# Kernel tuning notes

Hardware: AMD Instinct MI355X
Metric: run time of the kernel (lower is better)

## Reference

```python
import jax, jax.numpy as jnp
import numpy as np

B, S, NI = 8, 1024, 1024      # batch, seq_len, n_inputs
L, H, P = 128, 128, 64        # n_latents, hidden=n_inputs//8, prototype_dim
EPS_PROTO = 1e-4              # self.epsilon
BN_EPS = 1e-5                 # torch BatchNorm1d default eps


def setup_inputs() -> dict:
    key = jax.random.key(0)
    ks = jax.random.split(key, 4)
    return {
        "x": jax.random.normal(ks[0], (B, S, NI), jnp.float32),
        "W1": jax.random.normal(ks[1], (L, H, NI), jnp.float32) * 0.02,
        "b1": jnp.zeros((L, H), jnp.float32),
        "gamma": jnp.ones((L, H), jnp.float32),
        "beta": jnp.zeros((L, H), jnp.float32),
        "run_mean": jnp.zeros((L, H), jnp.float32),
        "run_var": jnp.ones((L, H), jnp.float32),
        "W2": jax.random.normal(ks[2], (L, P, H), jnp.float32) * 0.02,
        "b2": jnp.zeros((L, P), jnp.float32),
        "prototypes": jax.random.normal(ks[3], (L, P), jnp.float32) * 0.02,
    }


def reference(x, W1, b1, gamma, beta, run_mean, run_var, W2, b2, prototypes):
    Bb, Ss, _ = x.shape
    xf = x.reshape(Bb * Ss, NI)                       # [T, NI]
    # grouped first Linear over all latents at once: [T, L, H]
    h = jnp.einsum('ti,lhi->tlh', xf, W1) + b1
    # Dropout is identity in eval; BatchNorm1d in eval mode (running stats)
    h = (h - run_mean) * jax.lax.rsqrt(run_var + BN_EPS) * gamma + beta
    h = jax.nn.relu(h)
    # grouped second Linear: [T, L, P]
    enc = jnp.einsum('tlh,lph->tlp', h, W2) + b2
    # prototype L2-distance activation
    l2s = jnp.sum((enc - prototypes) ** 2, axis=-1)   # [T, L]
    raw = jnp.log((l2s + 1.0) / (l2s + EPS_PROTO))
    act = raw / jnp.log(1.0 / EPS_PROTO) * 300.0 - 100.0
    return act.reshape(Bb, Ss, L)
```

## Files before the change

kernel.cpp:

```cpp
#include <hip/hip_runtime.h>


#define NTOK 8192
#define NI   1024
#define NL   128
#define NH   128
#define NP   64

typedef __bf16 bf16x8 __attribute__((ext_vector_type(8)));
typedef float f32x4 __attribute__((ext_vector_type(4)));
typedef int   i32x4 __attribute__((ext_vector_type(4)));

static __device__ __forceinline__ unsigned short f2bf(float f) {
  union { float f; unsigned int u; } v; v.f = f;
  const unsigned int u = v.u;
  return (unsigned short)((u + 0x7fffu + ((u >> 16) & 1u)) >> 16);
}

__global__ void cvt_f32_bf16(const float* __restrict__ in,
                             unsigned short* __restrict__ out, int n8) {
  const int i = blockIdx.x * blockDim.x + threadIdx.x;
  if (i >= n8) return;
  const float4* p = (const float4*)in;
  const float4 a = p[2 * i], b = p[2 * i + 1];
  unsigned short v[8] __attribute__((aligned(16))) = {
      f2bf(a.x), f2bf(a.y), f2bf(a.z), f2bf(a.w),
      f2bf(b.x), f2bf(b.y), f2bf(b.z), f2bf(b.w)};
  ((uint4*)out)[i] = *(const uint4*)v;
}

__global__ void quant_rows_i8_dual(const float* __restrict__ x,
                                   const float* __restrict__ w1,
                                   signed char* __restrict__ xq,
                                   signed char* __restrict__ w1q,
                                   float* __restrict__ sx,
                                   float* __restrict__ sw) {
  const int row = blockIdx.x * 4 + (threadIdx.x >> 6);
  const int lane = threadIdx.x & 63;
  const float* src;
  unsigned int* dst;
  float* sp;
  if (row < NTOK) {
    src = x + (size_t)row * 1024;
    dst = (unsigned int*)(xq + (size_t)row * 1024);
    sp  = sx + row;
  } else {
    const int r = row - NTOK;
    src = w1 + (size_t)r * 1024;
    dst = (unsigned int*)(w1q + (size_t)r * 1024);
    sp  = sw + r;
  }
  const float4* s4 = (const float4*)src;
  float4 v[4];
  float m = 0.f;
#pragma unroll
  for (int j = 0; j < 4; ++j) {
    v[j] = s4[lane + 64 * j];
    m = fmaxf(m, fmaxf(fmaxf(fabsf(v[j].x), fabsf(v[j].y)),
                       fmaxf(fabsf(v[j].z), fabsf(v[j].w))));
  }
#pragma unroll
  for (int s = 1; s < 64; s <<= 1) m = fmaxf(m, __shfl_xor(m, s));
  m = fmaxf(m, 1e-20f);
  const float inv = 127.0f / m;
  if (lane == 0) *sp = m * (1.0f / 127.0f);
#pragma unroll
  for (int j = 0; j < 4; ++j) {
    const int a = (int)rintf(fminf(127.f, fmaxf(-127.f, v[j].x * inv)));
    const int b = (int)rintf(fminf(127.f, fmaxf(-127.f, v[j].y * inv)));
    const int c = (int)rintf(fminf(127.f, fmaxf(-127.f, v[j].z * inv)));
    const int d = (int)rintf(fminf(127.f, fmaxf(-127.f, v[j].w * inv)));
    dst[lane + 64 * j] = (unsigned)(a & 255) | ((unsigned)(b & 255) << 8) |
                         ((unsigned)(c & 255) << 16) | ((unsigned)(d & 255) << 24);
  }
}

static __device__ __forceinline__ void async16(const void* g, void* l) {
  __builtin_amdgcn_global_load_lds(
      (const __attribute__((address_space(1))) unsigned int*)g,
      (__attribute__((address_space(3))) unsigned int*)l, 16, 0, 0);
}

__global__ __launch_bounds__(256, 3) void proto_fused(
    const signed char* __restrict__ xq,
    const signed char* __restrict__ w1q,
    const unsigned short* __restrict__ w2b,
    const float* __restrict__ sx,
    const float* __restrict__ sw,
    const float* __restrict__ b1,
    const float* __restrict__ gamma, const float* __restrict__ beta,
    const float* __restrict__ rmean, const float* __restrict__ rvar,
    const float* __restrict__ b2,
    const float* __restrict__ protos,
    float* __restrict__ out)
{
  __shared__ __attribute__((aligned(128))) char smem[49152];
  const int tid  = threadIdx.x;
  const int wave = tid >> 6;
  const int lane = tid & 63;
  const int l15  = lane & 15;
  const int l4   = lane >> 4;
  const int wr   = wave >> 1;
  const int wc   = wave & 1;
  const int t0   = blockIdx.x * 128;
  const int lat  = blockIdx.y;

  const int srow  = lane >> 3;
  const int scolb = ((lane & 7) ^ srow) * 16;

  i32x4 acc[4][4] = {};

#pragma unroll
  for (int i = 0; i < 4; ++i) {
    const int r = wave * 4 + i * 16 + (lane >> 4);
    const int c = (lane & 15) ^ (r & 15);
    async16(w2b + (size_t)lat * NP * NH + r * NH + c * 8,
            smem + 32768 + (wave * 64 + i * 256) * 16);
  }

  auto stage = [&](int ks) {
    const int k0 = ks * 128;
#pragma unroll
    for (int j = 0; j < 4; ++j) {
      const int row = wave * 32 + j * 8 + srow;
      async16(xq + (size_t)(t0 + row) * NI + k0 + scolb,
              smem + (wave * 4 + j) * 1024);
      async16(w1q + (size_t)(lat * NH + row) * NI + k0 + scolb,
              smem + 16384 + (wave * 4 + j) * 1024);
    }
  };

  stage(0);
  const int rx = l15 & 7;
  for (int ks = 0; ks < 8; ++ks) {
    __syncthreads();
#pragma unroll
    for (int kk = 0; kk < 2; ++kk) {
      const int koff = ((kk * 4 + l4) ^ rx) << 4;
      i32x4 a[4], b[4];
#pragma unroll
      for (int m = 0; m < 4; ++m)
        a[m] = *(const i32x4*)(smem + (wr * 64 + m * 16 + l15) * 128 + koff);
#pragma unroll
      for (int n = 0; n < 4; ++n)
        b[n] = *(const i32x4*)(smem + 16384 + (wc * 64 + n * 16 + l15) * 128 + koff);
#pragma unroll
      for (int m = 0; m < 4; ++m)
#pragma unroll
        for (int n = 0; n < 4; ++n)
          acc[m][n] = __builtin_amdgcn_mfma_i32_16x16x64_i8(a[m], b[n], acc[m][n], 0, 0, 0);
    }
    __syncthreads();
    if (ks + 1 < 8) stage(ks + 1);
  }

  float sxv[4][4];
#pragma unroll
  for (int m = 0; m < 4; ++m)
#pragma unroll
    for (int r = 0; r < 4; ++r)
      sxv[m][r] = sx[t0 + wr * 64 + m * 16 + l4 * 4 + r];

#pragma unroll
  for (int n = 0; n < 4; ++n) {
    const int hc = wc * 64 + n * 16 + l15;
    const int gi = lat * NH + hc;
    const float sc_ = gamma[gi] * rsqrtf(rvar[gi] + 1e-5f);
    const float Kc  = sw[gi] * sc_;
    const float Cc  = b1[gi] * sc_ + beta[gi] - rmean[gi] * sc_;
    const int cchunk = hc >> 3, cin = (hc & 7) * 2;
#pragma unroll
    for (int m = 0; m < 4; ++m)
#pragma unroll
      for (int r = 0; r < 4; ++r) {
        float v = fmaf((float)acc[m][n][r] * sxv[m][r], Kc, Cc);
        v = v > 0.f ? v : 0.f;
        const int row = wr * 64 + m * 16 + l4 * 4 + r;
        const int pbyte = row * 256 + ((cchunk ^ (l4 * 4 + r)) << 4) + cin;
        *(__bf16*)(smem + pbyte) = (__bf16)v;
      }
  }
  __syncthreads();

  f32x4 acc2[2][4] = {};
#pragma unroll
  for (int kk = 0; kk < 4; ++kk) {
    const int pcsel = kk * 4 + l4;
    bf16x8 a2[2], bw[4];
#pragma unroll
    for (int m = 0; m < 2; ++m) {
      const int row = wave * 32 + m * 16 + l15;
      a2[m] = *(const bf16x8*)(smem + row * 256 + ((pcsel ^ (row & 15)) << 4));
    }
#pragma unroll
    for (int n = 0; n < 4; ++n) {
      const int rp = n * 16 + l15;
      bw[n] = *(const bf16x8*)(smem + 32768 + rp * 256 + ((pcsel ^ (rp & 15)) << 4));
    }
#pragma unroll
    for (int m = 0; m < 2; ++m)
#pragma unroll
      for (int n = 0; n < 4; ++n)
        acc2[m][n] = __builtin_amdgcn_mfma_f32_16x16x32_bf16(a2[m], bw[n], acc2[m][n], 0, 0, 0);
  }

  float pb[4], pp[4];
#pragma unroll
  for (int n = 0; n < 4; ++n) {
    const int p = n * 16 + l15;
    pb[n] = b2[lat * NP + p];
    pp[n] = protos[lat * NP + p];
  }
  const float scale2 = 0.69314718056f * 300.0f / logf(10000.0f);
#pragma unroll
  for (int m = 0; m < 2; ++m)
#pragma unroll
    for (int r = 0; r < 4; ++r) {
      float s = 0.f;
#pragma unroll
      for (int n = 0; n < 4; ++n) {
        const float e = acc2[m][n][r] + pb[n] - pp[n];
        s += e * e;
      }
      s += __shfl_xor(s, 1);
      s += __shfl_xor(s, 2);
      s += __shfl_xor(s, 4);
      s += __shfl_xor(s, 8);
      if (l15 == 0) {
        const float a = (__log2f(s + 1.0f) - __log2f(s + 1e-4f)) * scale2 - 100.0f;
        const int trow = wave * 32 + m * 16 + l4 * 4 + r;
        out[(size_t)(t0 + trow) * NL + lat] = a;
      }
    }
}

extern "C" void kernel_launch(void* const* d_in, const int* in_sizes, int n_in,
                              void* d_out, int out_size, void* d_ws, size_t ws_size,
                              hipStream_t stream) {
  const float* x      = (const float*)d_in[0];
  const float* W1     = (const float*)d_in[1];
  const float* b1     = (const float*)d_in[2];
  const float* gamma  = (const float*)d_in[3];
  const float* beta   = (const float*)d_in[4];
  const float* rmean  = (const float*)d_in[5];
  const float* rvar   = (const float*)d_in[6];
  const float* W2     = (const float*)d_in[7];
  const float* b2     = (const float*)d_in[8];
  const float* protos = (const float*)d_in[9];
  float* out = (float*)d_out;

  char* ws = (char*)d_ws;
  signed char*    xq  = (signed char*)ws;
  signed char*    w1q = (signed char*)(ws + (size_t)8 * 1024 * 1024);
  unsigned short* w2b = (unsigned short*)(ws + (size_t)24 * 1024 * 1024);
  float*          sx  = (float*)(ws + (size_t)26 * 1024 * 1024);
  float*          sw  = (float*)(ws + (size_t)26 * 1024 * 1024 + 64 * 1024);

  quant_rows_i8_dual<<<(NTOK + NL * NH) / 4, 256, 0, stream>>>(x, W1, xq, w1q, sx, sw);
  {
    const int n8w2 = NL * NP * NH / 8;
    cvt_f32_bf16<<<(n8w2 + 255) / 256, 256, 0, stream>>>(W2, w2b, n8w2);
  }

  dim3 grid(NTOK / 128, NL);
  proto_fused<<<grid, 256, 0, stream>>>(xq, w1q, w2b, sx, sw, b1, gamma, beta,
                                        rmean, rvar, b2, protos, out);
}
```

Before: 222.9 us.

## Load W2 directly from global, shrink LDS, remap blocks per XCD

Drops the 16KB LDS staging of W2 and has each lane read W2 bf16 fragments straight from global memory, prefetching one k-step ahead. This cuts shared memory to 32KB so occupancy can rise to 4 blocks per CU, and the launch bound is raised to match. The 2D grid becomes a 1D grid with a swizzle that keeps 16 latents per XCD and groups token tiles, so W1 and x tiles are reused in each XCD's L2. The cost is extra global/L2 traffic for W2 and more register pressure from the prefetch buffers.

```diff
diff --git a/kernel.cpp b/kernel.cpp
--- a/kernel.cpp
+++ b/kernel.cpp
@@ -81,7 +81,7 @@
       (__attribute__((address_space(3))) unsigned int*)l, 16, 0, 0);
 }
 
-__global__ __launch_bounds__(256, 3) void proto_fused(
+__global__ __launch_bounds__(256, 4) void proto_fused(
     const signed char* __restrict__ xq,
     const signed char* __restrict__ w1q,
     const unsigned short* __restrict__ w2b,
@@ -94,7 +94,7 @@
     const float* __restrict__ protos,
     float* __restrict__ out)
 {
-  __shared__ __attribute__((aligned(128))) char smem[49152];
+  __shared__ __attribute__((aligned(128))) char smem[32768];
   const int tid  = threadIdx.x;
   const int wave = tid >> 6;
   const int lane = tid & 63;
@@ -102,21 +102,20 @@
   const int l4   = lane >> 4;
   const int wr   = wave >> 1;
   const int wc   = wave & 1;
-  const int t0   = blockIdx.x * 128;
-  const int lat  = blockIdx.y;
+
+  const int id    = blockIdx.x;
+  const int xcd   = id & 7;
+  const int local = id >> 3;
+  const int chunk = local >> 7;
+  const int wi    = local & 127;
+  const int tt    = chunk * 8 + (wi & 7);
+  const int lat   = xcd * 16 + (wi >> 3);
+  const int t0    = tt * 128;
 
   const int srow  = lane >> 3;
   const int scolb = ((lane & 7) ^ srow) * 16;
 
   i32x4 acc[4][4] = {};
-
-#pragma unroll
-  for (int i = 0; i < 4; ++i) {
-    const int r = wave * 4 + i * 16 + (lane >> 4);
-    const int c = (lane & 15) ^ (r & 15);
-    async16(w2b + (size_t)lat * NP * NH + r * NH + c * 8,
-            smem + 32768 + (wave * 64 + i * 256) * 16);
-  }
 
   auto stage = [&](int ks) {
     const int k0 = ks * 128;
@@ -183,25 +182,32 @@
   __syncthreads();
 
   f32x4 acc2[2][4] = {};
+  const unsigned short* w2p = w2b + (size_t)lat * NP * NH + l15 * NH + l4 * 8;
+  bf16x8 bw[4], bwn[4];
+#pragma unroll
+  for (int n = 0; n < 4; ++n)
+    bw[n] = *(const bf16x8*)(w2p + n * 16 * NH);
 #pragma unroll
   for (int kk = 0; kk < 4; ++kk) {
+    if (kk < 3) {
+#pragma unroll
+      for (int n = 0; n < 4; ++n)
+        bwn[n] = *(const bf16x8*)(w2p + n * 16 * NH + (kk + 1) * 32);
+    }
     const int pcsel = kk * 4 + l4;
-    bf16x8 a2[2], bw[4];
+    bf16x8 a2[2];
 #pragma unroll
     for (int m = 0; m < 2; ++m) {
       const int row = wave * 32 + m * 16 + l15;
-      a2[m] = *(const bf16x8*)(smem + row * 256 + ((pcsel ^ (row & 15)) << 4));
-    }
-#pragma unroll
-    for (int n = 0; n < 4; ++n) {
-      const int rp = n * 16 + l15;
-      bw[n] = *(const bf16x8*)(smem + 32768 + rp * 256 + ((pcsel ^ (rp & 15)) << 4));
+      a2[m] = *(const bf16x8*)(smem + row * 256 + ((pcsel ^ l15) << 4));
     }
 #pragma unroll
     for (int m = 0; m < 2; ++m)
 #pragma unroll
       for (int n = 0; n < 4; ++n)
         acc2[m][n] = __builtin_amdgcn_mfma_f32_16x16x32_bf16(a2[m], bw[n], acc2[m][n], 0, 0, 0);
+#pragma unroll
+    for (int n = 0; n < 4; ++n) bw[n] = bwn[n];
   }
 
   float pb[4], pp[4];
@@ -262,7 +268,6 @@
     cvt_f32_bf16<<<(n8w2 + 255) / 256, 256, 0, stream>>>(W2, w2b, n8w2);
   }
 
-  dim3 grid(NTOK / 128, NL);
-  proto_fused<<<grid, 256, 0, stream>>>(xq, w1q, w2b, sx, sw, b1, gamma, beta,
-                                        rmean, rvar, b2, protos, out);
-}
+  proto_fused<<<dim3(8192), 256, 0, stream>>>(xq, w1q, w2b, sx, sw, b1, gamma, beta,
+                                              rmean, rvar, b2, protos, out);
+}
```

Result: slower. 239.0 us (+7.3%).
